# Kernel optimization log

Measured on AMD Instinct MI355X. Metric: run time of the kernel, lower is better.

## Reference

```python
import jax, jax.numpy as jnp
import numpy as np

D, H, FFN_D, B, LT, LS = 1024, 16, 4096, 4, 1024, 1024
EPS = 1e-5  # torch LayerNorm default
NEG = -10000000000.0


def setup_inputs() -> dict:
    key = jax.random.key(0)
    ks = iter(jax.random.split(key, 64))
    s = 0.02
    n = lambda shape: jax.random.normal(next(ks), shape, jnp.float32) * s
    inp = {
        'enc_output': n((LS, B, D)),
        'embedded': n((LT, B, D)),
        'src_mask': jnp.zeros((LS, B), jnp.bool_),
        'tgt_mask': jnp.zeros((LT, B), jnp.bool_),
    }
    for p in ('mmha', 'ed'):
        for w in ('q', 'k', 'v', 'o'):
            inp[f'{p}_w{w}'] = n((D, D))
            inp[f'{p}_b{w}'] = jnp.zeros((D,), jnp.float32)
    inp['ffn_w1'] = n((FFN_D, D)); inp['ffn_b1'] = jnp.zeros((FFN_D,), jnp.float32)
    inp['ffn_w2'] = n((D, FFN_D)); inp['ffn_b2'] = jnp.zeros((D,), jnp.float32)
    for i in range(3):
        inp[f'ln{i}_g'] = jnp.ones((D,), jnp.float32)
        inp[f'ln{i}_b'] = jnp.zeros((D,), jnp.float32)
    return inp


def _ln(x, g, b):
    m = x.mean(-1, keepdims=True)
    v = ((x - m) ** 2).mean(-1, keepdims=True)
    return (x - m) / jnp.sqrt(v + EPS) * g + b


def _mha(qx, kx, vx, wq, bq, wk, bk, wv, bv, wo, bo, mask):
    # qx: (Lq,B,D); kx,vx: (Lk,B,D); mask broadcastable to (B,H,Lq,Lk), True=masked
    Lq, Bn, Dm = qx.shape
    dk = Dm // H
    proj = lambda x, w, bb: (x @ w.T + bb).reshape(x.shape[0], Bn, H, dk).transpose(1, 2, 0, 3)
    q, k, v = proj(qx, wq, bq), proj(kx, wk, bk), proj(vx, wv, bv)  # (B,H,L,dk)
    scores = jnp.einsum('bhqd,bhkd->bhqk', q, k) / np.float32(np.sqrt(dk))
    scores = jnp.where(mask, NEG, scores)  # masked_fill semantics
    w = jax.nn.softmax(scores, axis=-1)  # dropout is identity in eval
    attn = jnp.einsum('bhqk,bhkd->bhqd', w, v).transpose(2, 0, 1, 3).reshape(Lq, Bn, Dm)
    return attn @ wo.T + bo


def reference(enc_output, embedded, src_mask, tgt_mask,
              mmha_wq, mmha_bq, mmha_wk, mmha_bk, mmha_wv, mmha_bv, mmha_wo, mmha_bo,
              ed_wq, ed_bq, ed_wk, ed_bk, ed_wv, ed_bv, ed_wo, ed_bo,
              ffn_w1, ffn_b1, ffn_w2, ffn_b2,
              ln0_g, ln0_b, ln1_g, ln1_b, ln2_g, ln2_b):
    Lt = embedded.shape[0]
    causal = jnp.triu(jnp.ones((Lt, Lt), jnp.bool_), 1)[None, None]      # (1,1,Lt,Lt)
    tmask = tgt_mask.T[:, None, None, :]                                  # (B,1,1,Lt)
    # Sublayer 0: masked self-attention (computed but UNUSED downstream,
    # faithfully mirroring the original forward which discards self_attn).
    self_attn = embedded + _mha(_ln(embedded, ln0_g, ln0_b), _ln(embedded, ln0_g, ln0_b), _ln(embedded, ln0_g, ln0_b),
                                mmha_wq, mmha_bq, mmha_wk, mmha_bk, mmha_wv, mmha_bv, mmha_wo, mmha_bo,
                                causal | tmask)
    del self_attn
    # Sublayer 1: enc-dec attention; residual input is `embedded` (as in source).
    smask = src_mask.T[:, None, None, :]                                  # (B,1,1,Ls)
    q_in = _ln(embedded, ln1_g, ln1_b)
    enc_dec = embedded + _mha(q_in, enc_output, enc_output,
                              ed_wq, ed_bq, ed_wk, ed_bk, ed_wv, ed_bv, ed_wo, ed_bo,
                              smask)
    # Sublayer 2: FFN
    z = _ln(enc_dec, ln2_g, ln2_b)
    ffn = jnp.maximum(z @ ffn_w1.T + ffn_b1, 0.0) @ ffn_w2.T + ffn_b2
    return enc_dec + ffn
```

## Files before the change

### kernel.cpp

```cpp
#include <hip/hip_runtime.h>
#include <cstdint>
#include <math.h>

constexpr int NH  = 16;
constexpr int DKH = 64;
constexpr int SEQ = 1024;
constexpr int NB  = 4;
constexpr int DM  = 1024;
constexpr int DF  = 4096;

typedef __bf16 bf16;
typedef __bf16 bf16x4 __attribute__((ext_vector_type(4)));
typedef __bf16 bf16x8 __attribute__((ext_vector_type(8)));
typedef float  f32x4  __attribute__((ext_vector_type(4)));

#define MFMA16(a, b, c) __builtin_amdgcn_mfma_f32_16x16x32_bf16((a), (b), (c), 0, 0, 0)

__device__ __forceinline__ void gload_lds16(const void* g, void* l) {
  __builtin_amdgcn_global_load_lds(
      (const __attribute__((address_space(1))) unsigned int*)(uintptr_t)g,
      (__attribute__((address_space(3))) unsigned int*)(uintptr_t)l,
      16, 0, 0);
}

template <int BK>
__device__ __forceinline__ int swz(int row) {
  return (BK == 32) ? ((row >> 1) & 3) : (row & 7);
}

template <int ROWS, int BK>
__device__ __forceinline__ void stage_tile(const bf16* __restrict__ g, int ldg,
                                           bf16* __restrict__ l, int t) {
  constexpr int ITER = ROWS * BK / 2048;
#pragma unroll
  for (int i = 0; i < ITER; ++i) {
    const int off = (i * 256 + t) * 8;
    const int row = off / BK;
    const int cc = (off & (BK - 1)) >> 3;
    const int sc = cc ^ swz<BK>(row);
    gload_lds16(&g[(size_t)row * ldg + (sc << 3)], &l[off]);
  }
}

__global__ __launch_bounds__(256) void prep_kernel(
    const float* __restrict__ wq, const float* __restrict__ wk,
    const float* __restrict__ wv, const float* __restrict__ wo,
    const float* __restrict__ w1, const float* __restrict__ w2,
    const float* __restrict__ enc, const float* __restrict__ emb,
    const float* __restrict__ g1, const float* __restrict__ be1,
    bf16* __restrict__ wqkv_bf, bf16* __restrict__ wo_bf,
    bf16* __restrict__ w1_bf, bf16* __restrict__ w2_bf,
    bf16* __restrict__ enc_bf, bf16* __restrict__ qin_bf) {
  const int bid = blockIdx.x, t = threadIdx.x;
  if (bid < 16384) {
    const float* in;
    bf16* out;
    int idx;
    if (bid < 4096) {
      const int sel = bid >> 10;
      in = sel == 0 ? wq : sel == 1 ? wk : sel == 2 ? wv : wo;
      out = sel == 3 ? wo_bf : wqkv_bf + ((size_t)sel << 20);
      idx = (bid & 1023) * 256 + t;
    } else {
      const int sel = (bid - 4096) >> 12;
      in = sel == 0 ? w1 : sel == 1 ? w2 : enc;
      out = sel == 0 ? w1_bf : sel == 1 ? w2_bf : enc_bf;
      idx = ((bid - 4096) & 4095) * 256 + t;
    }
    const float4 v = ((const float4*)in)[idx];
    bf16x4 ov;
    ov[0] = (bf16)v.x; ov[1] = (bf16)v.y; ov[2] = (bf16)v.z; ov[3] = (bf16)v.w;
    ((bf16x4*)out)[idx] = ov;
    return;
  }
  const int row = bid - 16384;
  const float4 v = ((const float4*)(emb + (size_t)row * DM))[t];
  float s  = v.x + v.y + v.z + v.w;
  float s2 = v.x * v.x + v.y * v.y + v.z * v.z + v.w * v.w;
#pragma unroll
  for (int m = 1; m < 64; m <<= 1) { s += __shfl_xor(s, m); s2 += __shfl_xor(s2, m); }
  __shared__ float red[8];
  const int w = t >> 6;
  if ((t & 63) == 0) { red[w] = s; red[4 + w] = s2; }
  __syncthreads();
  s  = red[0] + red[1] + red[2] + red[3];
  s2 = red[4] + red[5] + red[6] + red[7];
  const float mean = s * (1.f / DM);
  const float var  = s2 * (1.f / DM) - mean * mean;
  const float rstd = rsqrtf(var + 1e-5f);
  const float4 g4 = ((const float4*)g1)[t];
  const float4 b4 = ((const float4*)be1)[t];
  bf16x4 ov;
  ov[0] = (bf16)((v.x - mean) * rstd * g4.x + b4.x);
  ov[1] = (bf16)((v.y - mean) * rstd * g4.y + b4.y);
  ov[2] = (bf16)((v.z - mean) * rstd * g4.z + b4.z);
  ov[3] = (bf16)((v.w - mean) * rstd * g4.w + b4.w);
  ((bf16x4*)(qin_bf + (size_t)row * DM))[t] = ov;
}

__global__ __launch_bounds__(256) void ln_kernel(const float* __restrict__ x,
                                                 const float* __restrict__ gam,
                                                 const float* __restrict__ bet,
                                                 bf16* __restrict__ out) {
  const int row = blockIdx.x, t = threadIdx.x;
  const float4 v = ((const float4*)(x + (size_t)row * DM))[t];
  float s  = v.x + v.y + v.z + v.w;
  float s2 = v.x * v.x + v.y * v.y + v.z * v.z + v.w * v.w;
#pragma unroll
  for (int m = 1; m < 64; m <<= 1) { s += __shfl_xor(s, m); s2 += __shfl_xor(s2, m); }
  __shared__ float red[8];
  const int w = t >> 6;
  if ((t & 63) == 0) { red[w] = s; red[4 + w] = s2; }
  __syncthreads();
  s  = red[0] + red[1] + red[2] + red[3];
  s2 = red[4] + red[5] + red[6] + red[7];
  const float mean = s * (1.f / DM);
  const float var  = s2 * (1.f / DM) - mean * mean;
  const float rstd = rsqrtf(var + 1e-5f);
  const float4 g4 = ((const float4*)gam)[t];
  const float4 b4 = ((const float4*)bet)[t];
  bf16x4 ov;
  ov[0] = (bf16)((v.x - mean) * rstd * g4.x + b4.x);
  ov[1] = (bf16)((v.y - mean) * rstd * g4.y + b4.y);
  ov[2] = (bf16)((v.z - mean) * rstd * g4.z + b4.z);
  ov[3] = (bf16)((v.w - mean) * rstd * g4.w + b4.w);
  ((bf16x4*)(out + (size_t)row * DM))[t] = ov;
}

enum { EPI_QKV = 0, EPI_O = 3, EPI_F1 = 4, EPI_F2 = 5 };

struct GParams {
  const bf16* A;
  const bf16* A2;
  const bf16* W;
  const float* b0;
  const float* b1;
  const float* b2;
  const float* resid;
  void* out;
  void* out1;
  void* out2;
  int N;
  int K;
};

template <int MODE, int BN, int BK>
__global__ __launch_bounds__(256, 3) void gemm2(GParams p) {
  constexpr int BM = 128;
  constexpr int WTM = (BN == 128) ? 64 : 32;
  constexpr int MI = WTM / 16;
  __shared__ __align__(16) bf16 As[2][BM * BK];
  __shared__ __align__(16) bf16 Bs[2][BN * BK];
  const int t = threadIdx.x, lane = t & 63, w = t >> 6;
  const int lr = lane & 15, lg = lane >> 4;
  const int wr = (BN == 128) ? (w >> 1) : w;
  const int wc = (BN == 128) ? (w & 1) : 0;
  const int m0 = blockIdx.x * BM, n0 = blockIdx.y * BN;
  const bf16* Ap = (MODE == EPI_QKV && n0 >= 1024) ? p.A2 : p.A;
  const f32x4 FZ = {0.f, 0.f, 0.f, 0.f};
  f32x4 acc[MI][4];
#pragma unroll
  for (int i = 0; i < MI; ++i)
#pragma unroll
    for (int j = 0; j < 4; ++j) acc[i][j] = FZ;

  const int nk = p.K / BK;
  stage_tile<BM, BK>(&Ap[(size_t)m0 * p.K], p.K, As[0], t);
  stage_tile<BN, BK>(&p.W[(size_t)n0 * p.K], p.K, Bs[0], t);
  asm volatile("s_waitcnt vmcnt(0)" ::: "memory");
  __syncthreads();

  int cur = 0;
  for (int kt = 0; kt < nk; ++kt) {
    if (kt + 1 < nk) {
      stage_tile<BM, BK>(&Ap[(size_t)m0 * p.K + (size_t)(kt + 1) * BK], p.K, As[cur ^ 1], t);
      stage_tile<BN, BK>(&p.W[(size_t)n0 * p.K + (size_t)(kt + 1) * BK], p.K, Bs[cur ^ 1], t);
    }
    const bf16* Asl = As[cur];
    const bf16* Bsl = Bs[cur];
#pragma unroll
    for (int kh = 0; kh < BK / 32; ++kh) {
      bf16x8 af[MI], bfr[4];
#pragma unroll
      for (int i = 0; i < MI; ++i) {
        const int row = wr * WTM + i * 16 + lr;
        const int c = (kh * 4 + lg) ^ swz<BK>(row);
        af[i] = *(const bf16x8*)&Asl[row * BK + c * 8];
      }
#pragma unroll
      for (int j = 0; j < 4; ++j) {
        const int row = wc * 64 + j * 16 + lr;
        const int c = (kh * 4 + lg) ^ swz<BK>(row);
        bfr[j] = *(const bf16x8*)&Bsl[row * BK + c * 8];
      }
#pragma unroll
      for (int i = 0; i < MI; ++i)
#pragma unroll
        for (int j = 0; j < 4; ++j) acc[i][j] = MFMA16(af[i], bfr[j], acc[i][j]);
    }
    asm volatile("s_waitcnt vmcnt(0)" ::: "memory");
    __syncthreads();
    cur ^= 1;
  }

#pragma unroll
  for (int i = 0; i < MI; ++i) {
#pragma unroll
    for (int j = 0; j < 4; ++j) {
      const int c = n0 + wc * 64 + j * 16 + lr;
      float bj;
      if constexpr (MODE == EPI_QKV)
        bj = (c < 1024 ? p.b0 : c < 2048 ? p.b1 : p.b2)[c & 1023];
      else
        bj = p.b0[c];
#pragma unroll
      for (int g = 0; g < 4; ++g) {
        const int r = m0 + wr * WTM + i * 16 + 4 * lg + g;
        float v = acc[i][j][g] + bj;
        if constexpr (MODE == EPI_QKV) {
          const int cl = c & 1023;
          const size_t sidx = (((size_t)((r & 3) * NH + (cl >> 6)) << 10) + (r >> 2)) * DKH + (cl & 63);
          if (c < 1024)
            ((bf16*)p.out)[sidx] = (bf16)(v * 0.125f);
          else if (c < 2048)
            ((bf16*)p.out1)[sidx] = (bf16)v;
          else
            ((bf16*)p.out2)[(((size_t)((r & 3) * NH + (cl >> 6)) * DKH + (cl & 63)) << 10) + (r >> 2)] = (bf16)v;
        } else if constexpr (MODE == EPI_O) {
          const size_t idx = (size_t)r * p.N + c;
          ((float*)p.out)[idx] = v + p.resid[idx];
        } else if constexpr (MODE == EPI_F1) {
          ((bf16*)p.out)[(size_t)r * p.N + c] = (bf16)fmaxf(v, 0.f);
        } else {
          const size_t idx = (size_t)r * p.N + c;
          ((float*)p.out)[idx] = v + p.resid[idx];
        }
      }
    }
  }
}

__global__ __launch_bounds__(512, 4) void attn_kernel(const bf16* __restrict__ Qg,
                                                      const bf16* __restrict__ Kg,
                                                      const bf16* __restrict__ Vtg,
                                                      const unsigned char* __restrict__ smask,
                                                      bf16* __restrict__ Og) {
  __shared__ __align__(16) bf16 Ks[2][4096];
  __shared__ __align__(16) bf16 Vs[2][4096];
  __shared__ __align__(16) bf16 Ps[8][1152];
  const int t = threadIdx.x, lane = t & 63, w = t >> 6;
  const int lr = lane & 15, lg = lane >> 4;
  const int id = blockIdx.x;
  const int bh = ((id >> 6) << 3) | (id & 7);
  const int qt = (id >> 3) & 7;
  const int b = bh >> 4, h = bh & 15;
  const int q0 = qt * 128 + w * 16;
  const size_t base = (size_t)bh << 16;

  bf16x8 qa[2];
#pragma unroll
  for (int c = 0; c < 2; ++c)
    qa[c] = *(const bf16x8*)&Qg[base + (size_t)(q0 + lr) * DKH + c * 32 + lg * 8];

  const f32x4 FZ = {0.f, 0.f, 0.f, 0.f};
  f32x4 o[4];
  float mrun[4], lrun[4];
#pragma unroll
  for (int g = 0; g < 4; ++g) { mrun[g] = -INFINITY; lrun[g] = 0.f; o[g] = FZ; }

  const int soff = t * 8;
  const int shi = soff >> 11, smid = (soff >> 5) & 63;
  const int ssc = (((soff >> 3) & 3) ^ ((smid >> 1) & 3)) << 3;

  gload_lds16(&Kg[base + (size_t)smid * DKH + shi * 32 + ssc], &Ks[0][soff]);
  gload_lds16(&Vtg[base + (size_t)smid * SEQ + shi * 32 + ssc], &Vs[0][soff]);
  asm volatile("s_waitcnt vmcnt(0)" ::: "memory");
  __syncthreads();

  const int rsw = ((lr >> 1) & 3);

  int cur = 0;
  for (int kt = 0; kt < SEQ / 64; ++kt) {
    const int kv0 = kt * 64;
    if (kt + 1 < SEQ / 64) {
      gload_lds16(&Kg[base + (size_t)(kv0 + 64 + smid) * DKH + shi * 32 + ssc], &Ks[cur ^ 1][soff]);
      gload_lds16(&Vtg[base + (size_t)smid * SEQ + kv0 + 64 + shi * 32 + ssc], &Vs[cur ^ 1][soff]);
    }

    f32x4 s[4];
#pragma unroll
    for (int n = 0; n < 4; ++n) s[n] = FZ;
#pragma unroll
    for (int c = 0; c < 2; ++c) {
      bf16x8 kb[4];
#pragma unroll
      for (int n = 0; n < 4; ++n)
        kb[n] = *(const bf16x8*)&Ks[cur][c * 2048 + (n * 16 + lr) * 32 + ((lg ^ rsw) << 3)];
      __builtin_amdgcn_s_setprio(1);
#pragma unroll
      for (int n = 0; n < 4; ++n) s[n] = MFMA16(qa[c], kb[n], s[n]);
      __builtin_amdgcn_s_setprio(0);
    }

    float madd[4];
#pragma unroll
    for (int n = 0; n < 4; ++n)
      madd[n] = smask[(size_t)(kv0 + n * 16 + lr) * NB + b] ? -1e10f : 0.f;
#pragma unroll
    for (int n = 0; n < 4; ++n)
#pragma unroll
      for (int g = 0; g < 4; ++g) s[n][g] += madd[n];

    float tm4[4];
    bool needany = false;
#pragma unroll
    for (int g = 0; g < 4; ++g) {
      float tm = fmaxf(fmaxf(s[0][g], s[1][g]), fmaxf(s[2][g], s[3][g]));
      tm = fmaxf(tm, __shfl_xor(tm, 1));
      tm = fmaxf(tm, __shfl_xor(tm, 2));
      tm = fmaxf(tm, __shfl_xor(tm, 4));
      tm = fmaxf(tm, __shfl_xor(tm, 8));
      tm4[g] = tm;
      needany |= (tm > mrun[g] + 8.f);
    }
    if (__any(needany)) {
#pragma unroll
      for (int g = 0; g < 4; ++g) {
        const float mnew = fmaxf(mrun[g], tm4[g]);
        const float sc = __expf(mrun[g] - mnew);
        mrun[g] = mnew;
        lrun[g] *= sc;
#pragma unroll
        for (int n = 0; n < 4; ++n) o[n][g] *= sc;
      }
    }
#pragma unroll
    for (int g = 0; g < 4; ++g) {
      float ts = 0.f;
#pragma unroll
      for (int n = 0; n < 4; ++n) {
        const float p = __expf(s[n][g] - mrun[g]);
        s[n][g] = p;
        ts += p;
      }
      ts += __shfl_xor(ts, 1);
      ts += __shfl_xor(ts, 2);
      ts += __shfl_xor(ts, 4);
      ts += __shfl_xor(ts, 8);
      lrun[g] += ts;
    }

    bf16* Pw = &Ps[w][0];
#pragma unroll
    for (int n = 0; n < 4; ++n)
#pragma unroll
      for (int g = 0; g < 4; ++g)
        Pw[(4 * lg + g) * 72 + n * 16 + lr] = (bf16)s[n][g];
    __builtin_amdgcn_sched_barrier(0);

#pragma unroll
    for (int c = 0; c < 2; ++c) {
      const bf16x8 pa = *(const bf16x8*)&Pw[lr * 72 + c * 32 + lg * 8];
      bf16x8 vb[4];
#pragma unroll
      for (int n = 0; n < 4; ++n)
        vb[n] = *(const bf16x8*)&Vs[cur][c * 2048 + (n * 16 + lr) * 32 + ((lg ^ rsw) << 3)];
      __builtin_amdgcn_s_setprio(1);
#pragma unroll
      for (int n = 0; n < 4; ++n) o[n] = MFMA16(pa, vb[n], o[n]);
      __builtin_amdgcn_s_setprio(0);
    }

    asm volatile("s_waitcnt vmcnt(0)" ::: "memory");
    __syncthreads();
    cur ^= 1;
  }

#pragma unroll
  for (int g = 0; g < 4; ++g) {
    const int l = q0 + 4 * lg + g;
    const float inv = 1.0f / lrun[g];
#pragma unroll
    for (int n = 0; n < 4; ++n)
      Og[(size_t)(l * NB + b) * DM + h * 64 + n * 16 + lr] = (bf16)(o[n][g] * inv);
  }
}

extern "C" void kernel_launch(void* const* d_in, const int* in_sizes, int n_in,
                              void* d_out, int out_size, void* d_ws, size_t ws_size,
                              hipStream_t stream) {
  const float* enc = (const float*)d_in[0];
  const float* emb = (const float*)d_in[1];
  const unsigned char* smask = (const unsigned char*)d_in[2];
  const float* wq = (const float*)d_in[12]; const float* bq = (const float*)d_in[13];
  const float* wk = (const float*)d_in[14]; const float* bk = (const float*)d_in[15];
  const float* wv = (const float*)d_in[16]; const float* bv = (const float*)d_in[17];
  const float* wo = (const float*)d_in[18]; const float* bo = (const float*)d_in[19];
  const float* w1 = (const float*)d_in[20]; const float* b1 = (const float*)d_in[21];
  const float* w2 = (const float*)d_in[22]; const float* b2 = (const float*)d_in[23];
  const float* g1 = (const float*)d_in[26]; const float* be1 = (const float*)d_in[27];
  const float* g2 = (const float*)d_in[28]; const float* be2 = (const float*)d_in[29];

  char* ws = (char*)d_ws;
  const size_t MB = (size_t)1 << 20;
  bf16* wqkv_bf = (bf16*)(ws + 0 * MB);
  bf16* wo_bf   = (bf16*)(ws + 6 * MB);
  bf16* w1_bf   = (bf16*)(ws + 8 * MB);
  bf16* w2_bf   = (bf16*)(ws + 16 * MB);
  bf16* enc_bf  = (bf16*)(ws + 24 * MB);
  bf16* z_bf    = enc_bf;
  bf16* qin_bf  = (bf16*)(ws + 32 * MB);
  bf16* attn_bf = qin_bf;
  bf16* Q_bf    = (bf16*)(ws + 40 * MB);
  bf16* K_bf    = (bf16*)(ws + 48 * MB);
  bf16* Vt_bf   = (bf16*)(ws + 56 * MB);
  float* encdec = (float*)(ws + 64 * MB);
  bf16* h_bf    = (bf16*)(ws + 80 * MB);

  prep_kernel<<<20480, 256, 0, stream>>>(wq, wk, wv, wo, w1, w2, enc, emb, g1, be1,
                                         wqkv_bf, wo_bf, w1_bf, w2_bf, enc_bf, qin_bf);

  {
    GParams p{qin_bf, enc_bf, wqkv_bf, bq, bk, bv, nullptr, Q_bf, K_bf, Vt_bf, 3072, DM};
    gemm2<EPI_QKV, 128, 32><<<dim3(32, 24), 256, 0, stream>>>(p);
  }

  attn_kernel<<<512, 512, 0, stream>>>(Q_bf, K_bf, Vt_bf, smask, attn_bf);

  {
    GParams p{attn_bf, nullptr, wo_bf, bo, nullptr, nullptr, emb, encdec, nullptr, nullptr, DM, DM};
    gemm2<EPI_O, 64, 64><<<dim3(32, 16), 256, 0, stream>>>(p);
  }

  ln_kernel<<<4096, 256, 0, stream>>>(encdec, g2, be2, z_bf);

  {
    GParams p{z_bf, nullptr, w1_bf, b1, nullptr, nullptr, nullptr, h_bf, nullptr, nullptr, DF, DM};
    gemm2<EPI_F1, 128, 32><<<dim3(32, 32), 256, 0, stream>>>(p);
  }
  {
    GParams p{h_bf, nullptr, w2_bf, b2, nullptr, nullptr, encdec, d_out, nullptr, nullptr, DM, DF};
    gemm2<EPI_F2, 64, 64><<<dim3(32, 16), 256, 0, stream>>>(p);
  }
}
```

Before: 394.9 us.

## Deepen GEMM pipeline to 4-stage ring with partial vmcnt waits and LDS-staged epilogue

Replaces the double-buffered GEMM with a 4-slot LDS ring that prefetches two k-tiles ahead and waits with partial vmcnt counts before a single barrier per step, so loads overlap compute for longer. BK is fixed at 32 for all GEMMs, and s_setprio is raised around the MFMA block. For the QKV and FFN1 kernels, the epilogue now writes results into swizzled LDS and then stores them to global memory as 16-byte vectors, including the transposed V layout, instead of scattered 2-byte stores. The changes cost more LDS, which lowers occupancy (min blocks reduced to 2 for BN=128), and the BN=64 kernels get half the K-tile size they had before.

```diff
diff --git a/kernel.cpp b/kernel.cpp
--- a/kernel.cpp
+++ b/kernel.cpp
@@ -23,23 +23,33 @@
       16, 0, 0);
 }
 
-template <int BK>
-__device__ __forceinline__ int swz(int row) {
-  return (BK == 32) ? ((row >> 1) & 3) : (row & 7);
-}
-
-template <int ROWS, int BK>
-__device__ __forceinline__ void stage_tile(const bf16* __restrict__ g, int ldg,
-                                           bf16* __restrict__ l, int t) {
-  constexpr int ITER = ROWS * BK / 2048;
+template <int N>
+__device__ __forceinline__ void wait_vmcnt() {
+  if constexpr (N == 0)      asm volatile("s_waitcnt vmcnt(0)" ::: "memory");
+  else if constexpr (N == 3) asm volatile("s_waitcnt vmcnt(3)" ::: "memory");
+  else if constexpr (N == 4) asm volatile("s_waitcnt vmcnt(4)" ::: "memory");
+  else if constexpr (N == 6) asm volatile("s_waitcnt vmcnt(6)" ::: "memory");
+  else                       asm volatile("s_waitcnt vmcnt(8)" ::: "memory");
+}
+
+__device__ __forceinline__ int swz32(int row) { return (row >> 1) & 3; }
+
+template <int ROWS>
+__device__ __forceinline__ void stage_tile32(const bf16* __restrict__ g, int ldg,
+                                             bf16* __restrict__ l, int t) {
+  constexpr int ITER = ROWS * 32 / 2048;
 #pragma unroll
   for (int i = 0; i < ITER; ++i) {
     const int off = (i * 256 + t) * 8;
-    const int row = off / BK;
-    const int cc = (off & (BK - 1)) >> 3;
-    const int sc = cc ^ swz<BK>(row);
+    const int row = off >> 5;
+    const int cc = (off & 31) >> 3;
+    const int sc = cc ^ swz32(row);
     gload_lds16(&g[(size_t)row * ldg + (sc << 3)], &l[off]);
   }
+}
+
+__device__ __forceinline__ int rpk(int row, int col) {
+  return row * 256 + ((((col >> 3) ^ (row & 7)) << 4)) + ((col & 7) << 1);
 }
 
 __global__ __launch_bounds__(256) void prep_kernel(
@@ -144,19 +154,22 @@
   int K;
 };
 
-template <int MODE, int BN, int BK>
-__global__ __launch_bounds__(256, 3) void gemm2(GParams p) {
-  constexpr int BM = 128;
+template <int MODE, int BN, int MINB>
+__global__ __launch_bounds__(256, MINB) void gemm3(GParams p) {
+  constexpr int BM = 128, BK = 32;
   constexpr int WTM = (BN == 128) ? 64 : 32;
   constexpr int MI = WTM / 16;
-  __shared__ __align__(16) bf16 As[2][BM * BK];
-  __shared__ __align__(16) bf16 Bs[2][BN * BK];
+  constexpr int L = 2 + BN * BK / 2048;
+  __shared__ __align__(16) bf16 As[4][BM * BK];
+  __shared__ __align__(16) bf16 Bs[4][BN * BK];
   const int t = threadIdx.x, lane = t & 63, w = t >> 6;
   const int lr = lane & 15, lg = lane >> 4;
   const int wr = (BN == 128) ? (w >> 1) : w;
   const int wc = (BN == 128) ? (w & 1) : 0;
   const int m0 = blockIdx.x * BM, n0 = blockIdx.y * BN;
   const bf16* Ap = (MODE == EPI_QKV && n0 >= 1024) ? p.A2 : p.A;
+  const bf16* Wp = &p.W[(size_t)n0 * p.K];
+  const bf16* Arow = &Ap[(size_t)m0 * p.K];
   const f32x4 FZ = {0.f, 0.f, 0.f, 0.f};
   f32x4 acc[MI][4];
 #pragma unroll
@@ -165,49 +178,70 @@
     for (int j = 0; j < 4; ++j) acc[i][j] = FZ;
 
   const int nk = p.K / BK;
-  stage_tile<BM, BK>(&Ap[(size_t)m0 * p.K], p.K, As[0], t);
-  stage_tile<BN, BK>(&p.W[(size_t)n0 * p.K], p.K, Bs[0], t);
-  asm volatile("s_waitcnt vmcnt(0)" ::: "memory");
+  stage_tile32<BM>(Arow, p.K, As[0], t);
+  stage_tile32<BN>(Wp, p.K, Bs[0], t);
+  stage_tile32<BM>(Arow + BK, p.K, As[1], t);
+  stage_tile32<BN>(Wp + BK, p.K, Bs[1], t);
+
+  for (int kt = 0; kt < nk; ++kt) {
+    if (kt + 2 < nk) {
+      stage_tile32<BM>(Arow + (size_t)(kt + 2) * BK, p.K, As[(kt + 2) & 3], t);
+      stage_tile32<BN>(Wp + (size_t)(kt + 2) * BK, p.K, Bs[(kt + 2) & 3], t);
+      wait_vmcnt<2 * L>();
+    } else if (kt + 1 < nk) {
+      wait_vmcnt<L>();
+    } else {
+      wait_vmcnt<0>();
+    }
+    __builtin_amdgcn_s_barrier();
+
+    const bf16* Asl = As[kt & 3];
+    const bf16* Bsl = Bs[kt & 3];
+    bf16x8 af[MI], bfr[4];
+#pragma unroll
+    for (int i = 0; i < MI; ++i) {
+      const int row = wr * WTM + i * 16 + lr;
+      af[i] = *(const bf16x8*)&Asl[row * BK + ((lg ^ swz32(row)) << 3)];
+    }
+#pragma unroll
+    for (int j = 0; j < 4; ++j) {
+      const int row = wc * 64 + j * 16 + lr;
+      bfr[j] = *(const bf16x8*)&Bsl[row * BK + ((lg ^ swz32(row)) << 3)];
+    }
+    __builtin_amdgcn_s_setprio(1);
+#pragma unroll
+    for (int i = 0; i < MI; ++i)
+#pragma unroll
+      for (int j = 0; j < 4; ++j) acc[i][j] = MFMA16(af[i], bfr[j], acc[i][j]);
+    __builtin_amdgcn_s_setprio(0);
+  }
+
+  if constexpr (BN == 64) {
+#pragma unroll
+    for (int i = 0; i < MI; ++i) {
+#pragma unroll
+      for (int j = 0; j < 4; ++j) {
+        const int c = n0 + j * 16 + lr;
+        const float bj = p.b0[c];
+#pragma unroll
+        for (int g = 0; g < 4; ++g) {
+          const int r = m0 + wr * WTM + i * 16 + 4 * lg + g;
+          const size_t idx = (size_t)r * p.N + c;
+          ((float*)p.out)[idx] = acc[i][j][g] + bj + p.resid[idx];
+        }
+      }
+    }
+    return;
+  }
+
+  bf16* R = &As[0][0];
   __syncthreads();
-
-  int cur = 0;
-  for (int kt = 0; kt < nk; ++kt) {
-    if (kt + 1 < nk) {
-      stage_tile<BM, BK>(&Ap[(size_t)m0 * p.K + (size_t)(kt + 1) * BK], p.K, As[cur ^ 1], t);
-      stage_tile<BN, BK>(&p.W[(size_t)n0 * p.K + (size_t)(kt + 1) * BK], p.K, Bs[cur ^ 1], t);
-    }
-    const bf16* Asl = As[cur];
-    const bf16* Bsl = Bs[cur];
-#pragma unroll
-    for (int kh = 0; kh < BK / 32; ++kh) {
-      bf16x8 af[MI], bfr[4];
-#pragma unroll
-      for (int i = 0; i < MI; ++i) {
-        const int row = wr * WTM + i * 16 + lr;
-        const int c = (kh * 4 + lg) ^ swz<BK>(row);
-        af[i] = *(const bf16x8*)&Asl[row * BK + c * 8];
-      }
-#pragma unroll
-      for (int j = 0; j < 4; ++j) {
-        const int row = wc * 64 + j * 16 + lr;
-        const int c = (kh * 4 + lg) ^ swz<BK>(row);
-        bfr[j] = *(const bf16x8*)&Bsl[row * BK + c * 8];
-      }
-#pragma unroll
-      for (int i = 0; i < MI; ++i)
-#pragma unroll
-        for (int j = 0; j < 4; ++j) acc[i][j] = MFMA16(af[i], bfr[j], acc[i][j]);
-    }
-    asm volatile("s_waitcnt vmcnt(0)" ::: "memory");
-    __syncthreads();
-    cur ^= 1;
-  }
-
 #pragma unroll
   for (int i = 0; i < MI; ++i) {
 #pragma unroll
     for (int j = 0; j < 4; ++j) {
-      const int c = n0 + wc * 64 + j * 16 + lr;
+      const int col = wc * 64 + j * 16 + lr;
+      const int c = n0 + col;
       float bj;
       if constexpr (MODE == EPI_QKV)
         bj = (c < 1024 ? p.b0 : c < 2048 ? p.b1 : p.b2)[c & 1023];
@@ -215,26 +249,58 @@
         bj = p.b0[c];
 #pragma unroll
       for (int g = 0; g < 4; ++g) {
-        const int r = m0 + wr * WTM + i * 16 + 4 * lg + g;
+        const int row = wr * 64 + i * 16 + 4 * lg + g;
         float v = acc[i][j][g] + bj;
         if constexpr (MODE == EPI_QKV) {
-          const int cl = c & 1023;
-          const size_t sidx = (((size_t)((r & 3) * NH + (cl >> 6)) << 10) + (r >> 2)) * DKH + (cl & 63);
-          if (c < 1024)
-            ((bf16*)p.out)[sidx] = (bf16)(v * 0.125f);
-          else if (c < 2048)
-            ((bf16*)p.out1)[sidx] = (bf16)v;
-          else
-            ((bf16*)p.out2)[(((size_t)((r & 3) * NH + (cl >> 6)) * DKH + (cl & 63)) << 10) + (r >> 2)] = (bf16)v;
-        } else if constexpr (MODE == EPI_O) {
-          const size_t idx = (size_t)r * p.N + c;
-          ((float*)p.out)[idx] = v + p.resid[idx];
-        } else if constexpr (MODE == EPI_F1) {
-          ((bf16*)p.out)[(size_t)r * p.N + c] = (bf16)fmaxf(v, 0.f);
+          if (c < 1024) v *= 0.125f;
         } else {
-          const size_t idx = (size_t)r * p.N + c;
-          ((float*)p.out)[idx] = v + p.resid[idx];
+          v = fmaxf(v, 0.f);
         }
+        *(bf16*)((char*)R + rpk(row, col)) = (bf16)v;
+      }
+    }
+  }
+  __syncthreads();
+
+  if constexpr (MODE == EPI_F1) {
+#pragma unroll
+    for (int q = 0; q < 8; ++q) {
+      const int idx = q * 256 + t;
+      const int r = idx >> 4, cc = idx & 15;
+      const bf16x8 vv = *(const bf16x8*)((char*)R + r * 256 + (((cc ^ (r & 7)) << 4)));
+      *(bf16x8*)&((bf16*)p.out)[(size_t)(m0 + r) * p.N + n0 + cc * 8] = vv;
+    }
+  } else {
+    const int l0 = m0 >> 2;
+    const int h0 = (n0 & 1023) >> 6;
+    if (n0 < 2048) {
+      bf16* outp = (bf16*)(n0 < 1024 ? p.out : p.out1);
+#pragma unroll
+      for (int q = 0; q < 8; ++q) {
+        const int b = q >> 1, hsel = q & 1;
+        const int l = t >> 3, cc = t & 7;
+        const int row = l * 4 + b;
+        const int ccl = hsel * 8 + cc;
+        const bf16x8 vv = *(const bf16x8*)((char*)R + row * 256 + (((ccl ^ (row & 7)) << 4)));
+        const int bh = b * NH + h0 + hsel;
+        *(bf16x8*)&outp[(((size_t)bh << 10) + l0 + l) * DKH + cc * 8] = vv;
+      }
+    } else {
+      bf16* outp = (bf16*)p.out2;
+#pragma unroll
+      for (int q = 0; q < 8; ++q) {
+        const int idx = q * 256 + t;
+        const int rs = idx >> 2, kc = idx & 3;
+        const int b = rs >> 7, hsel = (rs >> 6) & 1, d = rs & 63;
+        const int col = hsel * 64 + d;
+        bf16x8 vv;
+#pragma unroll
+        for (int e = 0; e < 8; ++e) {
+          const int row = (kc * 8 + e) * 4 + b;
+          vv[e] = *(const bf16*)((char*)R + rpk(row, col));
+        }
+        const int bh = b * NH + h0 + hsel;
+        *(bf16x8*)&outp[(((size_t)bh * DKH + d) << 10) + l0 + kc * 8] = vv;
       }
     }
   }
@@ -422,24 +488,24 @@
 
   {
     GParams p{qin_bf, enc_bf, wqkv_bf, bq, bk, bv, nullptr, Q_bf, K_bf, Vt_bf, 3072, DM};
-    gemm2<EPI_QKV, 128, 32><<<dim3(32, 24), 256, 0, stream>>>(p);
+    gemm3<EPI_QKV, 128, 2><<<dim3(32, 24), 256, 0, stream>>>(p);
   }
 
   attn_kernel<<<512, 512, 0, stream>>>(Q_bf, K_bf, Vt_bf, smask, attn_bf);
 
   {
     GParams p{attn_bf, nullptr, wo_bf, bo, nullptr, nullptr, emb, encdec, nullptr, nullptr, DM, DM};
-    gemm2<EPI_O, 64, 64><<<dim3(32, 16), 256, 0, stream>>>(p);
+    gemm3<EPI_O, 64, 3><<<dim3(32, 16), 256, 0, stream>>>(p);
   }
 
   ln_kernel<<<4096, 256, 0, stream>>>(encdec, g2, be2, z_bf);
 
   {
     GParams p{z_bf, nullptr, w1_bf, b1, nullptr, nullptr, nullptr, h_bf, nullptr, nullptr, DF, DM};
-    gemm2<EPI_F1, 128, 32><<<dim3(32, 32), 256, 0, stream>>>(p);
+    gemm3<EPI_F1, 128, 2><<<dim3(32, 32), 256, 0, stream>>>(p);
   }
   {
     GParams p{h_bf, nullptr, w2_bf, b2, nullptr, nullptr, encdec, d_out, nullptr, nullptr, DM, DF};
-    gemm2<EPI_F2, 64, 64><<<dim3(32, 16), 256, 0, stream>>>(p);
-  }
-}
+    gemm3<EPI_F2, 64, 3><<<dim3(32, 16), 256, 0, stream>>>(p);
+  }
+}
```

Result: no change. 395.8 us (+0.2%).
